# Optimization experiments

Hardware: AMD Instinct MI355X
Metric: run time of the kernel (lower is better)

The kernel has to match this reference:

```python
import jax, jax.numpy as jnp
import numpy as np

N_HEADS = 32
N_KV_HEADS = 8
HEAD_DIM = 64
ROPE_THETA = 500000.0


def _rope_cos_sin(position_ids, head_dim, theta):
    # position_ids: [pb, S] int -> cos/sin [pb, S, head_dim]
    inv_freq = 1.0 / (theta ** (jnp.arange(0, head_dim, 2, dtype=jnp.float32) / head_dim))
    freqs = position_ids.astype(jnp.float32)[:, :, None] * inv_freq[None, None, :]  # [pb,S,D/2]
    emb = jnp.concatenate([freqs, freqs], axis=-1)  # [pb,S,D]
    return jnp.cos(emb), jnp.sin(emb)


def _rotate_half(x):
    d = x.shape[-1] // 2
    return jnp.concatenate([-x[..., d:], x[..., :d]], axis=-1)


def setup_inputs() -> dict:
    key = jax.random.key(0)
    k1, k2, k3, k4, k5 = jax.random.split(key, 5)
    B, S, H = 1, 2048, 2048
    KVD = N_KV_HEADS * HEAD_DIM
    scale = 0.02
    return {
        "hidden_states": jax.random.normal(k1, (B, S, H), jnp.float32),
        "position_ids": jnp.arange(S, dtype=jnp.int64 if jax.config.jax_enable_x64 else jnp.int32)[None, :],
        "Wq": jax.random.normal(k2, (H, H), jnp.float32) * scale,
        "Wk": jax.random.normal(k3, (H, KVD), jnp.float32) * scale,
        "Wv": jax.random.normal(k4, (H, KVD), jnp.float32) * scale,
        "Wo": jax.random.normal(k5, (H, H), jnp.float32) * scale,
    }


def reference(hidden_states, position_ids, Wq, Wk, Wv, Wo):
    B, S, H = hidden_states.shape
    G = N_HEADS // N_KV_HEADS  # GQA group size

    q = (hidden_states @ Wq).reshape(B, S, N_HEADS, HEAD_DIM).transpose(0, 2, 1, 3)      # [B,Hq,S,D]
    k = (hidden_states @ Wk).reshape(B, S, N_KV_HEADS, HEAD_DIM).transpose(0, 2, 1, 3)   # [B,Hk,S,D]
    v = (hidden_states @ Wv).reshape(B, S, N_KV_HEADS, HEAD_DIM).transpose(0, 2, 1, 3)   # [B,Hk,S,D]

    cos, sin = _rope_cos_sin(position_ids, HEAD_DIM, ROPE_THETA)  # [pb,S,D]
    cos = cos[:, None].astype(hidden_states.dtype)  # [pb,1,S,D] broadcasts over heads
    sin = sin[:, None].astype(hidden_states.dtype)
    q = q * cos + _rotate_half(q) * sin
    k = k * cos + _rotate_half(k) * sin

    # GQA without materializing repeated K/V: group query heads by kv head
    qg = q.reshape(B, N_KV_HEADS, G, S, HEAD_DIM)
    scale = 1.0 / jnp.sqrt(jnp.asarray(HEAD_DIM, hidden_states.dtype))
    scores = jnp.einsum('bkgqd,bksd->bkgqs', qg, k) * scale  # [B,Hk,G,S,S]
    causal = jnp.tril(jnp.ones((S, S), bool))
    scores = jnp.where(causal, scores, jnp.asarray(-jnp.inf, scores.dtype))
    probs = jax.nn.softmax(scores, axis=-1)
    out = jnp.einsum('bkgqs,bksd->bkgqd', probs, v)  # [B,Hk,G,S,D]
    out = out.reshape(B, N_HEADS, S, HEAD_DIM).transpose(0, 2, 1, 3).reshape(B, S, H)
    return out @ Wo
```

## Files before the change

### kernel.cpp

```cpp
#include <hip/hip_runtime.h>
#include <hip/hip_bf16.h>
#include <math.h>

#define S_LEN 2048
#define HID   2048
#define NH    32
#define NKV   8
#define HD    64
#define QKD   2560
#define LOG2E 1.44269504f
#define L2THETA_32 0.591611505f

typedef unsigned short u16;
typedef __attribute__((ext_vector_type(8))) short short8;
typedef __attribute__((ext_vector_type(4))) float f32x4;

__device__ __forceinline__ u16 f2bf(float x) {
    union { __hip_bfloat16 b; u16 u; } c; c.b = __float2bfloat16(x); return c.u;
}
__device__ __forceinline__ float bf2f(u16 u) {
    union { unsigned int i; float f; } c; c.i = ((unsigned int)u) << 16; return c.f;
}
__device__ __forceinline__ void async_copy16(void* lds, const void* g) {
    __builtin_amdgcn_global_load_lds((const __attribute__((address_space(1))) unsigned int*)g,
                                     (__attribute__((address_space(3))) unsigned int*)lds,
                                     16, 0, 0);
}

__global__ __launch_bounds__(256)
void cast_bf16(const float* __restrict__ in, u16* __restrict__ out, int n8) {
    int i = blockIdx.x * blockDim.x + threadIdx.x;
    if (i >= n8) return;
    const float4* p = (const float4*)(in + (size_t)i * 8);
    float4 a = p[0], b = p[1];
    short8 o;
    o[0] = f2bf(a.x); o[1] = f2bf(a.y); o[2] = f2bf(a.z); o[3] = f2bf(a.w);
    o[4] = f2bf(b.x); o[5] = f2bf(b.y); o[6] = f2bf(b.z); o[7] = f2bf(b.w);
    *(short8*)(out + (size_t)i * 8) = o;
}

__global__ __launch_bounds__(256)
void transpose_all(const float* __restrict__ Wq, const float* __restrict__ Wk,
                   const float* __restrict__ Wv, const float* __restrict__ Wo,
                   u16* __restrict__ WqkvT, u16* __restrict__ WoT) {
    const float* W; u16* WT; int Nin, xT;
    switch (blockIdx.z) {
        case 0:  W = Wq; WT = WqkvT;                         Nin = 2048; xT = 64; break;
        case 1:  W = Wk; WT = WqkvT + (size_t)2048 * 2048;   Nin = 512;  xT = 16; break;
        case 2:  W = Wv; WT = WqkvT + (size_t)2560 * 2048;   Nin = 512;  xT = 16; break;
        default: W = Wo; WT = WoT;                           Nin = 2048; xT = 64; break;
    }
    if ((int)blockIdx.x >= xT) return;
    __shared__ float tile[32][33];
    const int tx = threadIdx.x & 31, ty = threadIdx.x >> 5;
    const int x = blockIdx.x * 32 + tx;
#pragma unroll
    for (int j = ty; j < 32; j += 8)
        tile[j][tx] = W[(size_t)(blockIdx.y * 32 + j) * Nin + x];
    __syncthreads();
    const int xo = blockIdx.y * 32 + tx;
#pragma unroll
    for (int j = ty; j < 32; j += 8)
        WT[(size_t)(blockIdx.x * 32 + j) * 2048 + xo] = f2bf(tile[tx][j]);
}

__global__ __launch_bounds__(256)
void rope_qk(u16* __restrict__ QK, const int* __restrict__ pos) {
    int idx = blockIdx.x * blockDim.x + threadIdx.x;
    int d = idx & 31;
    int hh = (idx >> 5) % 40;
    int s = idx / (32 * 40);
    if (s >= S_LEN) return;
    float p = (float)pos[s];
    float inv_freq = exp2f(-(float)d * L2THETA_32);
    float ang = p * inv_freq;
    float c = cosf(ang), sn = sinf(ang);
    float sc = (hh < 32) ? 0.125f * LOG2E : 1.0f;
    u16* b = QK + (size_t)s * QKD + hh * HD;
    float x0 = bf2f(b[d]), x1 = bf2f(b[d + 32]);
    b[d]      = f2bf((x0 * c - x1 * sn) * sc);
    b[d + 32] = f2bf((x1 * c + x0 * sn) * sc);
}

template<int MODE>
__global__ __launch_bounds__(512)
void gemm_bt(const u16* __restrict__ A, const u16* __restrict__ Bt,
             void* __restrict__ Cv, u16* __restrict__ Vt, int M, int N, int K) {
    __shared__ __attribute__((aligned(16))) u16 As[2][4096];
    __shared__ __attribute__((aligned(16))) u16 Bs[2][4096];
    const int t = threadIdx.x;
    const int lane = t & 63;
    const int w = t >> 6;
    const int lm = lane & 15, quad = lane >> 4;
    const int row0 = blockIdx.y * 128, col0 = blockIdx.x * 128;
    const int wr = (w >> 1) * 32, wc = (w & 1) * 64;

    f32x4 acc[2][4];
#pragma unroll
    for (int i = 0; i < 2; ++i)
#pragma unroll
        for (int j = 0; j < 4; ++j) acc[i][j] = (f32x4){0.f, 0.f, 0.f, 0.f};

    const size_t strideB = (size_t)K * 2;
    const char* Ab = (const char*)(A + (size_t)row0 * K);
    const char* Bb = (const char*)(Bt + (size_t)col0 * K);

    auto stage = [&](int k0, int buf) {
        const int f = t * 16;
        const int r = f >> 6, cb = f & 63;
        async_copy16((char*)As[buf] + f, Ab + (size_t)r * strideB + k0 * 2 + cb);
        async_copy16((char*)Bs[buf] + f, Bb + (size_t)r * strideB + k0 * 2 + cb);
    };

    const int nk = K >> 5;
    stage(0, 0);
    if (nk > 1) stage(32, 1);

    for (int kk = 0; kk < nk; ++kk) {
        const int cur = kk & 1;
        if (kk + 1 < nk) { asm volatile("s_waitcnt vmcnt(2)\ns_barrier" ::: "memory"); }
        else             { asm volatile("s_waitcnt vmcnt(0)\ns_barrier" ::: "memory"); }

        short8 af[2], bfv[4];
#pragma unroll
        for (int i = 0; i < 2; ++i)
            af[i] = *(const short8*)((const char*)As[cur] + (wr + 16 * i + lm) * 64 + quad * 16);
#pragma unroll
        for (int j = 0; j < 4; ++j)
            bfv[j] = *(const short8*)((const char*)Bs[cur] + (wc + 16 * j + lm) * 64 + quad * 16);
#pragma unroll
        for (int i = 0; i < 2; ++i)
#pragma unroll
            for (int j = 0; j < 4; ++j)
                acc[i][j] = __builtin_amdgcn_mfma_f32_16x16x32_bf16(af[i], bfv[j], acc[i][j], 0, 0, 0);

        asm volatile("s_waitcnt lgkmcnt(0)\ns_barrier" ::: "memory");
        if (kk + 2 < nk) stage((kk + 2) * 32, cur);
    }

    const int cr = quad * 4;
#pragma unroll
    for (int i = 0; i < 2; ++i) {
        const int gr = row0 + wr + 16 * i + cr;
#pragma unroll
        for (int j = 0; j < 4; ++j) {
            const int gc = col0 + wc + 16 * j + lm;
            if (MODE == 0) {
#pragma unroll
                for (int rr = 0; rr < 4; ++rr)
                    ((float*)Cv)[(size_t)(gr + rr) * N + gc] = acc[i][j][rr];
            } else if (gc < 2560) {
#pragma unroll
                for (int rr = 0; rr < 4; ++rr)
                    ((u16*)Cv)[(size_t)(gr + rr) * QKD + gc] = f2bf(acc[i][j][rr]);
            } else {
                const int d = gc - 2560;
                ushort4 vv;
                vv.x = f2bf(acc[i][j][0]); vv.y = f2bf(acc[i][j][1]);
                vv.z = f2bf(acc[i][j][2]); vv.w = f2bf(acc[i][j][3]);
                *(ushort4*)(Vt + (size_t)d * S_LEN + gr) = vv;
            }
        }
    }
}

__global__ __launch_bounds__(256)
void attn_mfma(const u16* __restrict__ QK, const u16* __restrict__ Vtg,
               u16* __restrict__ Ctx) {
    __shared__ __attribute__((aligned(16))) u16 QPs[4096];
    __shared__ __attribute__((aligned(16))) u16 Ks[2][4096];
    __shared__ __attribute__((aligned(16))) u16 Vts[2][4096];

    const int t = threadIdx.x;
    const int lane = t & 63;
    const int w = t >> 6;
    const int lm = lane & 15, quad = lane >> 4;
    const int qt = (gridDim.x - 1) - blockIdx.x;
    const int h = blockIdx.y;
    const int kh = h >> 2;
    const int q0 = qt * 64;
    const int njt = qt + 1;

    const char* Kb = (const char*)(QK + 2048 + kh * HD);
    const char* Vb = (const char*)(Vtg + (size_t)(kh * 64) * S_LEN);

    const int srow = t >> 3;
    const int scswz = ((t & 7) ^ (srow & 7)) * 16;

    {
        const char* qb = (const char*)(QK + h * HD);
        const int qrow = w * 16 + (lane >> 3);
        const int qcs = ((lane & 7) ^ (lane >> 3)) * 16;
#pragma unroll
        for (int k2 = 0; k2 < 2; ++k2)
            async_copy16((char*)QPs + w * 2048 + k2 * 1024 + lane * 16,
                         qb + (size_t)(q0 + qrow + k2 * 8) * (QKD * 2) + qcs);
    }

    auto stage_kv = [&](int jt_, int buf) {
        const int j0_ = jt_ * 64;
        char* kdst = (char*)Ks + buf * 8192 + t * 16;
        char* vdst = (char*)Vts + buf * 8192 + t * 16;
        async_copy16(kdst,        Kb + (size_t)(j0_ + srow)      * (QKD * 2) + scswz);
        async_copy16(kdst + 4096, Kb + (size_t)(j0_ + 32 + srow) * (QKD * 2) + scswz);
        async_copy16(vdst,        Vb + (size_t)srow        * (S_LEN * 2) + j0_ * 2 + scswz);
        async_copy16(vdst + 4096, Vb + (size_t)(32 + srow) * (S_LEN * 2) + j0_ * 2 + scswz);
    };

    stage_kv(0, 0);
    if (njt > 1) {
        stage_kv(1, 1);
        asm volatile("s_waitcnt vmcnt(8)" ::: "memory");
    } else {
        asm volatile("s_waitcnt vmcnt(4)" ::: "memory");
    }

    const int ra = w * 16 + lm;
    const int fswz = ((quad ^ (lm & 7)) << 4);
    const short8 qa0 = *(const short8*)((const char*)QPs + ra * 128 + fswz);
    const short8 qa1 = *(const short8*)((const char*)QPs + ra * 128 + (fswz ^ 64));
    asm volatile("s_waitcnt lgkmcnt(0)" ::: "memory");

    short8 onesf;
    {
        const short ob = (lm == 0) ? (short)0x3F80 : (short)0;
#pragma unroll
        for (int j = 0; j < 8; ++j) onesf[j] = ob;
    }

    f32x4 oa[4], la;
#pragma unroll
    for (int dt = 0; dt < 4; ++dt) oa[dt] = (f32x4){0.f, 0.f, 0.f, 0.f};
    la = (f32x4){0.f, 0.f, 0.f, 0.f};

    for (int jt = 0; jt < njt; ++jt) {
        const int cur = jt & 1;
        if (jt + 1 < njt) { asm volatile("s_waitcnt vmcnt(4)\ns_barrier" ::: "memory"); }
        else              { asm volatile("s_waitcnt vmcnt(0)\ns_barrier" ::: "memory"); }

        const char* Kc = (const char*)Ks + cur * 8192;
        const char* Vc = (const char*)Vts + cur * 8192;

        f32x4 sa[4];
#pragma unroll
        for (int ct = 0; ct < 4; ++ct)
            sa[ct] = (f32x4){-16.f, -16.f, -16.f, -16.f};
#pragma unroll
        for (int ct = 0; ct < 4; ++ct) {
            const char* kr = Kc + (ct * 16 + lm) * 128;
            short8 kf0 = *(const short8*)(kr + fswz);
            short8 kf1 = *(const short8*)(kr + (fswz ^ 64));
            sa[ct] = __builtin_amdgcn_mfma_f32_16x16x32_bf16(kf0, qa0, sa[ct], 0, 0, 0);
            sa[ct] = __builtin_amdgcn_mfma_f32_16x16x32_bf16(kf1, qa1, sa[ct], 0, 0, 0);
        }
        if (jt == qt) {
#pragma unroll
            for (int ct = 0; ct < 4; ++ct) {
                const int kvl = ct * 16 + quad * 4;
#pragma unroll
                for (int r = 0; r < 4; ++r)
                    if (kvl + r > ra) sa[ct][r] = -1e30f;
            }
        }
#pragma unroll
        for (int ct = 0; ct < 4; ++ct) {
            ushort4 pka;
            pka.x = f2bf(__builtin_amdgcn_exp2f(sa[ct][0]));
            pka.y = f2bf(__builtin_amdgcn_exp2f(sa[ct][1]));
            pka.z = f2bf(__builtin_amdgcn_exp2f(sa[ct][2]));
            pka.w = f2bf(__builtin_amdgcn_exp2f(sa[ct][3]));
            const int pc = (((2 * ct + (quad >> 1)) ^ (lm & 7)) << 4) + ((quad & 1) << 3);
            *(ushort4*)((char*)QPs + ra * 128 + pc) = pka;
        }
        const short8 pa0 = *(const short8*)((const char*)QPs + ra * 128 + fswz);
        const short8 pa1 = *(const short8*)((const char*)QPs + ra * 128 + (fswz ^ 64));
#pragma unroll
        for (int dt = 0; dt < 4; ++dt) {
            const char* vr = Vc + (dt * 16 + lm) * 128;
            short8 vf0 = *(const short8*)(vr + fswz);
            short8 vf1 = *(const short8*)(vr + (fswz ^ 64));
            oa[dt] = __builtin_amdgcn_mfma_f32_16x16x32_bf16(vf0, pa0, oa[dt], 0, 0, 0);
            oa[dt] = __builtin_amdgcn_mfma_f32_16x16x32_bf16(vf1, pa1, oa[dt], 0, 0, 0);
        }
        la = __builtin_amdgcn_mfma_f32_16x16x32_bf16(onesf, pa0, la, 0, 0, 0);
        la = __builtin_amdgcn_mfma_f32_16x16x32_bf16(onesf, pa1, la, 0, 0, 0);

        asm volatile("s_waitcnt lgkmcnt(0)\ns_barrier" ::: "memory");
        if (jt + 2 < njt) stage_kv(jt + 2, cur);
    }

    const float inva = 1.f / __shfl(la[0], lm);
    const int rowa = q0 + ra;
#pragma unroll
    for (int dt = 0; dt < 4; ++dt) {
        ushort4 o;
        o.x = f2bf(oa[dt][0] * inva); o.y = f2bf(oa[dt][1] * inva);
        o.z = f2bf(oa[dt][2] * inva); o.w = f2bf(oa[dt][3] * inva);
        *(ushort4*)(Ctx + (size_t)rowa * HID + h * HD + dt * 16 + quad * 4) = o;
    }
}

extern "C" void kernel_launch(void* const* d_in, const int* in_sizes, int n_in,
                              void* d_out, int out_size, void* d_ws, size_t ws_size,
                              hipStream_t stream) {
    const float* X   = (const float*)d_in[0];
    const int*   pos = (const int*)d_in[1];
    const float* Wq  = (const float*)d_in[2];
    const float* Wk  = (const float*)d_in[3];
    const float* Wv  = (const float*)d_in[4];
    const float* Wo  = (const float*)d_in[5];
    float* out = (float*)d_out;

    u16* Xb    = (u16*)d_ws;
    u16* WqkvT = Xb + (size_t)4194304;
    u16* WoT   = WqkvT + (size_t)6291456;
    u16* QK    = WoT + (size_t)4194304;
    u16* Vt    = QK + (size_t)S_LEN * QKD;
    u16* Ctxb  = Xb;

    cast_bf16<<<2048, 256, 0, stream>>>(X, Xb, 524288);
    transpose_all<<<dim3(64, 64, 4), 256, 0, stream>>>(Wq, Wk, Wv, Wo, WqkvT, WoT);

    gemm_bt<1><<<dim3(24, 16), 512, 0, stream>>>(Xb, WqkvT, QK, Vt, 2048, 3072, 2048);

    rope_qk<<<10240, 256, 0, stream>>>(QK, pos);

    attn_mfma<<<dim3(32, 32), 256, 0, stream>>>(QK, Vt, Ctxb);

    gemm_bt<0><<<dim3(16, 16), 512, 0, stream>>>(Ctxb, WoT, out, nullptr, 2048, 2048, 2048);
}
```

Measured before the change: 251.0 us.

## Retile GEMM to 128x64 blocks with BK=64 and XOR-swizzled LDS

The bf16 GEMM goes from 128x128 tiles with 512 threads and a K-step of 32 to 128x64 tiles with 256 threads and a K-step of 64. Each wave now owns a 32-row strip across the full 64 columns. LDS rows are 128 bytes, and the 16-byte chunk index is XOR-swizzled with the row on both stage and fragment loads to avoid bank conflicts. This aims to halve the barrier count per K, double the grid size for better CU fill on the small GEMMs, and remove LDS conflicts. The cost is more B-tile reloads per output and a larger A buffer.

```diff
diff --git a/kernel.cpp b/kernel.cpp
--- a/kernel.cpp
+++ b/kernel.cpp
@@ -83,17 +83,17 @@
 }
 
 template<int MODE>
-__global__ __launch_bounds__(512)
+__global__ __launch_bounds__(256)
 void gemm_bt(const u16* __restrict__ A, const u16* __restrict__ Bt,
              void* __restrict__ Cv, u16* __restrict__ Vt, int M, int N, int K) {
-    __shared__ __attribute__((aligned(16))) u16 As[2][4096];
+    __shared__ __attribute__((aligned(16))) u16 As[2][8192];
     __shared__ __attribute__((aligned(16))) u16 Bs[2][4096];
     const int t = threadIdx.x;
     const int lane = t & 63;
     const int w = t >> 6;
     const int lm = lane & 15, quad = lane >> 4;
-    const int row0 = blockIdx.y * 128, col0 = blockIdx.x * 128;
-    const int wr = (w >> 1) * 32, wc = (w & 1) * 64;
+    const int row0 = blockIdx.y * 128, col0 = blockIdx.x * 64;
+    const int wr = w * 32;
 
     f32x4 acc[2][4];
 #pragma unroll
@@ -105,37 +105,55 @@
     const char* Ab = (const char*)(A + (size_t)row0 * K);
     const char* Bb = (const char*)(Bt + (size_t)col0 * K);
 
-    auto stage = [&](int k0, int buf) {
-        const int f = t * 16;
-        const int r = f >> 6, cb = f & 63;
-        async_copy16((char*)As[buf] + f, Ab + (size_t)r * strideB + k0 * 2 + cb);
-        async_copy16((char*)Bs[buf] + f, Bb + (size_t)r * strideB + k0 * 2 + cb);
+    const int srow = t >> 3;
+    const int scswz = ((t & 7) ^ (srow & 7)) * 16;
+
+    auto stage = [&](int ks, int buf) {
+        const int k0b = ks * 128;
+        char* ad = (char*)As[buf] + t * 16;
+        char* bd = (char*)Bs[buf] + t * 16;
+#pragma unroll
+        for (int i = 0; i < 4; ++i)
+            async_copy16(ad + i * 4096, Ab + (size_t)(i * 32 + srow) * strideB + k0b + scswz);
+#pragma unroll
+        for (int i = 0; i < 2; ++i)
+            async_copy16(bd + i * 4096, Bb + (size_t)(i * 32 + srow) * strideB + k0b + scswz);
     };
 
-    const int nk = K >> 5;
+    const int nk = K >> 6;
     stage(0, 0);
-    if (nk > 1) stage(32, 1);
+    if (nk > 1) stage(1, 1);
+
+    const int fswz = (quad ^ (lm & 7)) << 4;
 
     for (int kk = 0; kk < nk; ++kk) {
         const int cur = kk & 1;
-        if (kk + 1 < nk) { asm volatile("s_waitcnt vmcnt(2)\ns_barrier" ::: "memory"); }
+        if (kk + 1 < nk) { asm volatile("s_waitcnt vmcnt(6)\ns_barrier" ::: "memory"); }
         else             { asm volatile("s_waitcnt vmcnt(0)\ns_barrier" ::: "memory"); }
 
-        short8 af[2], bfv[4];
+        short8 af[2][2], bfv[4][2];
+#pragma unroll
+        for (int i = 0; i < 2; ++i) {
+            const char* ar = (const char*)As[cur] + (wr + 16 * i + lm) * 128;
+            af[i][0] = *(const short8*)(ar + fswz);
+            af[i][1] = *(const short8*)(ar + (fswz ^ 64));
+        }
+#pragma unroll
+        for (int j = 0; j < 4; ++j) {
+            const char* br = (const char*)Bs[cur] + (16 * j + lm) * 128;
+            bfv[j][0] = *(const short8*)(br + fswz);
+            bfv[j][1] = *(const short8*)(br + (fswz ^ 64));
+        }
 #pragma unroll
         for (int i = 0; i < 2; ++i)
-            af[i] = *(const short8*)((const char*)As[cur] + (wr + 16 * i + lm) * 64 + quad * 16);
-#pragma unroll
-        for (int j = 0; j < 4; ++j)
-            bfv[j] = *(const short8*)((const char*)Bs[cur] + (wc + 16 * j + lm) * 64 + quad * 16);
-#pragma unroll
-        for (int i = 0; i < 2; ++i)
-#pragma unroll
-            for (int j = 0; j < 4; ++j)
-                acc[i][j] = __builtin_amdgcn_mfma_f32_16x16x32_bf16(af[i], bfv[j], acc[i][j], 0, 0, 0);
+#pragma unroll
+            for (int j = 0; j < 4; ++j) {
+                acc[i][j] = __builtin_amdgcn_mfma_f32_16x16x32_bf16(af[i][0], bfv[j][0], acc[i][j], 0, 0, 0);
+                acc[i][j] = __builtin_amdgcn_mfma_f32_16x16x32_bf16(af[i][1], bfv[j][1], acc[i][j], 0, 0, 0);
+            }
 
         asm volatile("s_waitcnt lgkmcnt(0)\ns_barrier" ::: "memory");
-        if (kk + 2 < nk) stage((kk + 2) * 32, cur);
+        if (kk + 2 < nk) stage(kk + 2, cur);
     }
 
     const int cr = quad * 4;
@@ -144,7 +162,7 @@
         const int gr = row0 + wr + 16 * i + cr;
 #pragma unroll
         for (int j = 0; j < 4; ++j) {
-            const int gc = col0 + wc + 16 * j + lm;
+            const int gc = col0 + 16 * j + lm;
             if (MODE == 0) {
 #pragma unroll
                 for (int rr = 0; rr < 4; ++rr)
@@ -321,11 +339,11 @@
     cast_bf16<<<2048, 256, 0, stream>>>(X, Xb, 524288);
     transpose_all<<<dim3(64, 64, 4), 256, 0, stream>>>(Wq, Wk, Wv, Wo, WqkvT, WoT);
 
-    gemm_bt<1><<<dim3(24, 16), 512, 0, stream>>>(Xb, WqkvT, QK, Vt, 2048, 3072, 2048);
+    gemm_bt<1><<<dim3(48, 16), 256, 0, stream>>>(Xb, WqkvT, QK, Vt, 2048, 3072, 2048);
 
     rope_qk<<<10240, 256, 0, stream>>>(QK, pos);
 
     attn_mfma<<<dim3(32, 32), 256, 0, stream>>>(QK, Vt, Ctxb);
 
-    gemm_bt<0><<<dim3(16, 16), 512, 0, stream>>>(Ctxb, WoT, out, nullptr, 2048, 2048, 2048);
-}
+    gemm_bt<0><<<dim3(32, 16), 256, 0, stream>>>(Ctxb, WoT, out, nullptr, 2048, 2048, 2048);
+}
```

Result: faster. 230.2 us (-8.3%).
